# Kernel optimization log

Hardware: AMD Instinct MI355X
Metric: run time of the kernel (lower is better)

## Reference

```python
import jax, jax.numpy as jnp
import numpy as np

N_NODES = 16384
N_EDGES = 32768
D = 128          # node feature / hidden dim
EDGE_DIM = 10    # bond featurizer one-hot dim
EH = 32          # edge_hidden_dim in the NNConv MLPs


def _nnconv(x, src, dst, edge_attr, l1w, l1b, l2w, l2b, root, bias):
    """PyG NNConv with aggr='mean': out_i = x_i @ root + mean_{e: dst=i} x_{src_e} @ W(e) + bias."""
    E = edge_attr.shape[0]
    h = jax.nn.relu(edge_attr @ l1w + l1b)              # [E, EH]
    W = (h @ l2w + l2b).reshape(E, D, D)                # per-edge weight matrices [E, D, D]
    msg = jnp.einsum('ei,eio->eo', x[src], W)           # gather + per-edge matmul [E, D]
    s = jax.ops.segment_sum(msg, dst, num_segments=N_NODES)
    cnt = jax.ops.segment_sum(jnp.ones((E, 1), x.dtype), dst, num_segments=N_NODES)
    agg = s / jnp.maximum(cnt, 1.0)                     # scatter-mean (0 for isolated nodes)
    return x @ root + agg + bias


def setup_inputs() -> dict:
    key = jax.random.key(0)
    ks = jax.random.split(key, 14)
    x = jax.random.normal(ks[0], (N_NODES, D), dtype=jnp.float32)
    edge_index = jax.random.randint(ks[1], (2, N_EDGES), 0, N_NODES, dtype=jnp.int64)
    edge_attr = jax.random.uniform(ks[2], (N_EDGES, EDGE_DIM), dtype=jnp.float32)

    def lin(k, fan_in, fan_out):
        return jax.random.normal(k, (fan_in, fan_out), dtype=jnp.float32) / np.sqrt(fan_in)

    return {
        'x': x, 'edge_index': edge_index, 'edge_attr': edge_attr,
        # subgraph_conv1 (128 -> 128)
        'w1_l1': lin(ks[3], EDGE_DIM, EH), 'b1_l1': jnp.zeros((EH,), jnp.float32),
        'w1_l2': lin(ks[4], EH, D * D),    'b1_l2': jnp.zeros((D * D,), jnp.float32),
        'w1_root': lin(ks[5], D, D),       'b1': jnp.zeros((D,), jnp.float32),
        # subgraph_conv2 (128 -> 128), applied twice with shared weights
        'w2_l1': lin(ks[6], EDGE_DIM, EH), 'b2_l1': jnp.zeros((EH,), jnp.float32),
        'w2_l2': lin(ks[7], EH, D * D),    'b2_l2': jnp.zeros((D * D,), jnp.float32),
        'w2_root': lin(ks[8], D, D),       'b2': jnp.zeros((D,), jnp.float32),
    }


def reference(x, edge_index, edge_attr,
              w1_l1, b1_l1, w1_l2, b1_l2, w1_root, b1,
              w2_l1, b2_l1, w2_l2, b2_l2, w2_root, b2):
    src, dst = edge_index[0], edge_index[1]
    h = jax.nn.relu(_nnconv(x, src, dst, edge_attr, w1_l1, b1_l1, w1_l2, b1_l2, w1_root, b1))
    h = jax.nn.relu(_nnconv(h, src, dst, edge_attr, w2_l1, b2_l1, w2_l2, b2_l2, w2_root, b2))
    h = _nnconv(h, src, dst, edge_attr, w2_l1, b2_l1, w2_l2, b2_l2, w2_root, b2)
    return h
```

## Files before the change

### kernel.cpp

```cpp
#include <hip/hip_runtime.h>

#define N_NODES 16384
#define N_EDGES 32768
#define D 128
#define EDGE_DIM 10
#define KH 32
#define BM 128
#define XST2 72
#define XST 136
#define NBL 32

typedef _Float16 f16;
typedef _Float16 f16x4 __attribute__((ext_vector_type(4)));
typedef _Float16 f16x8 __attribute__((ext_vector_type(8)));
typedef float f32x4 __attribute__((ext_vector_type(4)));

__global__ __launch_bounds__(256) void deg_pack_kernel(
    const int* __restrict__ ei, int* __restrict__ deg,
    const float* __restrict__ w1l2, const float* __restrict__ w2l2,
    const float* __restrict__ b1l2, const float* __restrict__ b2l2,
    const float* __restrict__ rt1, const float* __restrict__ rt2,
    f16* __restrict__ Bp1, f16* __restrict__ Bp2,
    f16* __restrict__ Rp1, f16* __restrict__ Rp2) {
  int y = blockIdx.y;
  if (y == 0) {
    int e = blockIdx.x * 256 + threadIdx.x;
    if (e < N_EDGES) atomicAdd(&deg[ei[N_EDGES + e]], 1);
    return;
  }
  if (blockIdx.x >= D * D / 256) return;
  int t = blockIdx.x * 256 + threadIdx.x;
  int j = y - 1;
  if (j < 2) {
    const float* l2w = j ? w2l2 : w1l2;
    f16* Bp = j ? Bp2 : Bp1;
    f16 tmp[KH];
#pragma unroll
    for (int k = 0; k < KH; k++) tmp[k] = (f16)l2w[(size_t)k * (D * D) + t];
    f16x8* dst = (f16x8*)(Bp + (size_t)t * KH);
#pragma unroll
    for (int c = 0; c < 4; c++) dst[c] = *(f16x8*)&tmp[c * 8];
  } else {
    const float* src = (j == 2) ? b1l2 : (j == 3) ? b2l2 : (j == 4) ? rt1 : rt2;
    f16* dst = (j == 2) ? (Bp1 + (size_t)D * D * KH)
             : (j == 3) ? (Bp2 + (size_t)D * D * KH)
             : (j == 4) ? Rp1 : Rp2;
    int i = t >> 7, o = t & 127;
    dst[((size_t)(i >> 5) * D + o) * KH + (i & 31)] = (f16)src[t];
  }
}

__global__ __launch_bounds__(1024) void scan_kernel(
    const int* __restrict__ deg, int* __restrict__ rs, int* __restrict__ fill) {
  __shared__ int part[1024];
  int t = threadIdx.x;
  int base = t * 16;
  int loc[16], s = 0;
#pragma unroll
  for (int j = 0; j < 16; j++) { loc[j] = deg[base + j]; s += loc[j]; }
  part[t] = s;
  __syncthreads();
  for (int off = 1; off < 1024; off <<= 1) {
    int add = (t >= off) ? part[t - off] : 0;
    __syncthreads();
    part[t] += add;
    __syncthreads();
  }
  int run = t ? part[t - 1] : 0;
#pragma unroll
  for (int j = 0; j < 16; j++) {
    rs[base + j] = run; fill[base + j] = run; run += loc[j];
  }
  if (t == 1023) rs[N_NODES] = run;
}

__global__ __launch_bounds__(256) void scatter_kernel(
    const int* __restrict__ ei, int* __restrict__ fill,
    int* __restrict__ perm, int* __restrict__ srcs) {
  int e = blockIdx.x * blockDim.x + threadIdx.x;
  if (e < N_EDGES) {
    int pos = atomicAdd(&fill[ei[N_EDGES + e]], 1);
    perm[pos] = e;
    srcs[pos] = ei[e];
  }
}

__global__ __launch_bounds__(256) void xcvt_kernel(
    const float* __restrict__ xin, f16* __restrict__ xh) {
  int t = blockIdx.x * 256 + threadIdx.x;
  const float4* s = (const float4*)(xin + (size_t)t * 8);
  float4 v0 = s[0], v1 = s[1];
  f16x8 h = {(f16)v0.x, (f16)v0.y, (f16)v0.z, (f16)v0.w,
             (f16)v1.x, (f16)v1.y, (f16)v1.z, (f16)v1.w};
  *(f16x8*)(xh + (size_t)t * 8) = h;
}

__global__ __launch_bounds__(256) void edge_mlp_kernel(
    const float* __restrict__ ea, const int* __restrict__ perm,
    const float* __restrict__ w1l1, const float* __restrict__ b1l1,
    const float* __restrict__ w2l1, const float* __restrict__ b2l1,
    f16* __restrict__ h1, f16* __restrict__ h2) {
  int p = blockIdx.x * blockDim.x + threadIdx.x;
  const float* l1w = blockIdx.y ? w2l1 : w1l1;
  const float* l1b = blockIdx.y ? b2l1 : b1l1;
  f16* h = blockIdx.y ? h2 : h1;
  int e = perm[p];
  float a[EDGE_DIM];
#pragma unroll
  for (int d = 0; d < EDGE_DIM; d++) a[d] = ea[e * EDGE_DIM + d];
  f16 hv[KH];
#pragma unroll
  for (int k = 0; k < KH; k++) {
    float acc = l1b[k];
#pragma unroll
    for (int d = 0; d < EDGE_DIM; d++) acc += a[d] * l1w[d * KH + k];
    hv[k] = (f16)fmaxf(acc, 0.0f);
  }
  f16x8* dst = (f16x8*)(h + (size_t)p * KH);
#pragma unroll
  for (int c = 0; c < 4; c++) dst[c] = *(f16x8*)&hv[c * 8];
}

__global__ __launch_bounds__(256, 2) void msg_mfma_kernel(
    const f16* __restrict__ xh, const f16* __restrict__ hf,
    const f16* __restrict__ Bp, const int* __restrict__ srcs,
    f16* __restrict__ msgfA, f16* __restrict__ msgfB) {
  __shared__ f16 Xs[BM][XST2];
  __shared__ f16 Hs[BM][KH];
  int t = threadIdx.x;
  int e0 = blockIdx.x * BM;
  int y  = blockIdx.y;
  f16* msgf = y ? msgfB : msgfA;

  ((f16x8*)Hs)[t]       = ((const f16x8*)(hf + (size_t)e0 * KH))[t];
  ((f16x8*)Hs)[t + 256] = ((const f16x8*)(hf + (size_t)e0 * KH))[t + 256];
  {
    int r = t >> 1, q = t & 1;
    int s = srcs[e0 + r];
    const float4* src = (const float4*)(xh + (size_t)s * D + y * 64 + q * 32);
    float4* dst = (float4*)&Xs[r][q * 32];
#pragma unroll
    for (int c = 0; c < 4; c++) dst[c] = src[c];
  }

  int L = t & 63, w = t >> 6;
  int quad = L >> 4, lm = L & 15;
  int n0 = w * 32;

  const f16* bl = Bp + ((size_t)(y * 64) * D + n0 + lm) * KH + quad * 8;
  const size_t istr = (size_t)D * KH;

  f32x4 acc[8][2];
#pragma unroll
  for (int mt = 0; mt < 8; mt++)
#pragma unroll
    for (int nt = 0; nt < 2; nt++)
      acc[mt][nt] = (f32x4){0.f, 0.f, 0.f, 0.f};

  f16x8 bufA[4][2], bufB[4][2];

  auto loadg = [&](f16x8 (&buf)[4][2], int basei) {
#pragma unroll
    for (int jj = 0; jj < 4; jj++) {
      const f16* bi = bl + (size_t)(basei + jj) * istr;
      buf[jj][0] = *(const f16x8*)bi;
      buf[jj][1] = *(const f16x8*)(bi + 16 * KH);
    }
  };

  f16x8 hreg[8];

  auto compute = [&](f16x8 (&buf)[4][2], int ig) {
    f16x4 xv[8];
#pragma unroll
    for (int mt = 0; mt < 8; mt++)
      xv[mt] = *(const f16x4*)&Xs[mt * 16 + lm][ig];
#pragma unroll
    for (int jj = 0; jj < 4; jj++) {
#pragma unroll
      for (int mt = 0; mt < 8; mt++) {
        f16 xs = xv[mt][jj];
        f16x8 xb = {xs, xs, xs, xs, xs, xs, xs, xs};
        f16x8 a = hreg[mt] * xb;
        acc[mt][0] = __builtin_amdgcn_mfma_f32_16x16x32_f16(a, buf[jj][0], acc[mt][0], 0, 0, 0);
        acc[mt][1] = __builtin_amdgcn_mfma_f32_16x16x32_f16(a, buf[jj][1], acc[mt][1], 0, 0, 0);
      }
    }
  };

  loadg(bufA, 0);
  __syncthreads();

#pragma unroll
  for (int mt = 0; mt < 8; mt++)
    hreg[mt] = *(const f16x8*)&Hs[mt * 16 + lm][quad * 8];

#pragma unroll 1
  for (int g = 0; g < 8; g++) {
    loadg(bufB, 8 * g + 4);
    compute(bufA, 8 * g);
    loadg(bufA, 8 * g + 8);
    compute(bufB, 8 * g + 4);
  }

  {
    const f16* bb = Bp + (size_t)D * D * KH;
#pragma unroll
    for (int g2 = 0; g2 < 2; g2++) {
      int ig2 = 2 * y + g2;
      const f16* b2l = bb + ((size_t)ig2 * D + n0 + lm) * KH + quad * 8;
      f16x8 b0 = *(const f16x8*)b2l;
      f16x8 b1 = *(const f16x8*)(b2l + 16 * KH);
      int lc = g2 * 32 + quad * 8;
#pragma unroll
      for (int mt = 0; mt < 8; mt++) {
        f16x8 a = *(const f16x8*)&Xs[mt * 16 + lm][lc];
        acc[mt][0] = __builtin_amdgcn_mfma_f32_16x16x32_f16(a, b0, acc[mt][0], 0, 0, 0);
        acc[mt][1] = __builtin_amdgcn_mfma_f32_16x16x32_f16(a, b1, acc[mt][1], 0, 0, 0);
      }
    }
  }

#pragma unroll
  for (int mt = 0; mt < 8; mt++)
#pragma unroll
    for (int r = 0; r < 4; r++) {
      f16* mg = msgf + (size_t)(e0 + mt * 16 + quad * 4 + r) * D + n0 + lm;
      mg[0]  = (f16)acc[mt][0][r];
      mg[16] = (f16)acc[mt][1][r];
    }
}

__global__ __launch_bounds__(256) void node_update_kernel(
    const f16* __restrict__ xh, const f16* __restrict__ msgA,
    const f16* __restrict__ msgB, const int* __restrict__ rs,
    const f16* __restrict__ Rp, const float* __restrict__ bias,
    f16* __restrict__ xout, float* __restrict__ fout, int is_final) {
  __shared__ f16 Xs[NBL][XST];
  __shared__ float Sls[NBL][D];
  int t = threadIdx.x;
  int nb = blockIdx.x * NBL;

  {
    int r = t >> 3, q = t & 7;
    const float4* src = (const float4*)(xh + (size_t)(nb + r) * D + q * 16);
    float4* dst = (float4*)&Xs[r][q * 16];
    dst[0] = src[0];
    dst[1] = src[1];
  }
  __syncthreads();

  {
    int nl = t >> 3, o0 = (t & 7) * 16;
    int n = nb + nl;
    int a = rs[n], b = rs[n + 1];
    float sum[16];
#pragma unroll
    for (int j = 0; j < 16; j++) sum[j] = 0.f;
    for (int r = a; r < b; r++) {
      f16x8 a0 = *(const f16x8*)(msgA + (size_t)r * D + o0);
      f16x8 a1 = *(const f16x8*)(msgA + (size_t)r * D + o0 + 8);
      f16x8 b0 = *(const f16x8*)(msgB + (size_t)r * D + o0);
      f16x8 b1 = *(const f16x8*)(msgB + (size_t)r * D + o0 + 8);
#pragma unroll
      for (int j = 0; j < 8; j++) {
        sum[j]     += (float)a0[j] + (float)b0[j];
        sum[8 + j] += (float)a1[j] + (float)b1[j];
      }
    }
    float inv = 1.0f / (float)max(b - a, 1);
#pragma unroll
    for (int j = 0; j < 16; j++) Sls[nl][o0 + j] = sum[j] * inv;
  }
  __syncthreads();

  int L = t & 63, w = t >> 6;
  int quad = L >> 4, lm = L & 15;
  int n0 = w * 32;
  f32x4 acc[2][2];
#pragma unroll
  for (int mt = 0; mt < 2; mt++)
#pragma unroll
    for (int nt = 0; nt < 2; nt++)
      acc[mt][nt] = (f32x4){0.f, 0.f, 0.f, 0.f};
#pragma unroll
  for (int s4 = 0; s4 < 4; s4++) {
    const f16* b2l = Rp + ((size_t)s4 * D + n0 + lm) * KH + quad * 8;
    f16x8 b0 = *(const f16x8*)b2l;
    f16x8 b1 = *(const f16x8*)(b2l + 16 * KH);
#pragma unroll
    for (int mt = 0; mt < 2; mt++) {
      f16x8 a = *(const f16x8*)&Xs[mt * 16 + lm][s4 * 32 + quad * 8];
      acc[mt][0] = __builtin_amdgcn_mfma_f32_16x16x32_f16(a, b0, acc[mt][0], 0, 0, 0);
      acc[mt][1] = __builtin_amdgcn_mfma_f32_16x16x32_f16(a, b1, acc[mt][1], 0, 0, 0);
    }
  }
#pragma unroll
  for (int mt = 0; mt < 2; mt++)
#pragma unroll
    for (int r = 0; r < 4; r++) {
      Sls[mt * 16 + quad * 4 + r][n0 + lm] += acc[mt][0][r];
      Sls[mt * 16 + quad * 4 + r][n0 + 16 + lm] += acc[mt][1][r];
    }
  __syncthreads();

  {
    int o = t & 127, g = t >> 7;
    float bo = bias[o];
    if (is_final) {
      for (int q = g * 16; q < g * 16 + 16; q++)
        fout[(size_t)(nb + q) * D + o] = bo + Sls[q][o];
    } else {
      for (int q = g * 16; q < g * 16 + 16; q++)
        xout[(size_t)(nb + q) * D + o] = (f16)fmaxf(bo + Sls[q][o], 0.0f);
    }
  }
}

extern "C" void kernel_launch(void* const* d_in, const int* in_sizes, int n_in,
                              void* d_out, int out_size, void* d_ws, size_t ws_size,
                              hipStream_t stream) {
  const float* x      = (const float*)d_in[0];
  const int*   ei     = (const int*)d_in[1];
  const float* ea     = (const float*)d_in[2];
  const float* w1_l1  = (const float*)d_in[3];
  const float* b1_l1  = (const float*)d_in[4];
  const float* w1_l2  = (const float*)d_in[5];
  const float* b1_l2  = (const float*)d_in[6];
  const float* w1_rt  = (const float*)d_in[7];
  const float* b1     = (const float*)d_in[8];
  const float* w2_l1  = (const float*)d_in[9];
  const float* b2_l1  = (const float*)d_in[10];
  const float* w2_l2  = (const float*)d_in[11];
  const float* b2_l2  = (const float*)d_in[12];
  const float* w2_rt  = (const float*)d_in[13];
  const float* b2     = (const float*)d_in[14];
  float* out = (float*)d_out;

  const size_t BPSZ = (size_t)D * D * KH + (size_t)D * D + 32768;
  f16* h1f = (f16*)d_ws;
  f16* h2f = h1f + (size_t)N_EDGES * KH;
  f16* Bp1 = h2f + (size_t)N_EDGES * KH;
  f16* Bp2 = Bp1 + BPSZ;
  f16* Rp1 = Bp2 + BPSZ;
  f16* Rp2 = Rp1 + (size_t)D * D;
  int* deg  = (int*)(Rp2 + (size_t)D * D);
  int* rs   = deg + N_NODES;
  int* fill = rs + N_NODES + 128;
  int* perm = fill + N_NODES;
  int* srcs = perm + N_EDGES;
  f16* msgA = (f16*)(srcs + N_EDGES);
  f16* msgB = msgA + (size_t)N_EDGES * D;
  f16* xh0  = msgB + (size_t)N_EDGES * D;
  f16* xh1  = xh0 + (size_t)N_NODES * D;

  hipMemsetAsync(deg, 0, N_NODES * sizeof(int), stream);
  deg_pack_kernel<<<dim3(N_EDGES / 256, 7), 256, 0, stream>>>(
      ei, deg, w1_l2, w2_l2, b1_l2, b2_l2, w1_rt, w2_rt, Bp1, Bp2, Rp1, Rp2);
  scan_kernel<<<1, 1024, 0, stream>>>(deg, rs, fill);
  scatter_kernel<<<N_EDGES / 256, 256, 0, stream>>>(ei, fill, perm, srcs);
  edge_mlp_kernel<<<dim3(N_EDGES / 256, 2), 256, 0, stream>>>(
      ea, perm, w1_l1, b1_l1, w2_l1, b2_l1, h1f, h2f);
  xcvt_kernel<<<N_NODES * D / (256 * 8), 256, 0, stream>>>(x, xh0);

  msg_mfma_kernel<<<dim3(N_EDGES / BM, 2), 256, 0, stream>>>(xh0, h1f, Bp1, srcs, msgA, msgB);
  node_update_kernel<<<N_NODES / NBL, 256, 0, stream>>>(xh0, msgA, msgB, rs, Rp1, b1, xh1, out, 0);
  msg_mfma_kernel<<<dim3(N_EDGES / BM, 2), 256, 0, stream>>>(xh1, h2f, Bp2, srcs, msgA, msgB);
  node_update_kernel<<<N_NODES / NBL, 256, 0, stream>>>(xh1, msgA, msgB, rs, Rp2, b2, xh0, out, 0);
  msg_mfma_kernel<<<dim3(N_EDGES / BM, 2), 256, 0, stream>>>(xh0, h2f, Bp2, srcs, msgA, msgB);
  node_update_kernel<<<N_NODES / NBL, 256, 0, stream>>>(xh0, msgA, msgB, rs, Rp2, b2, (f16*)nullptr, out, 1);
}
```

Baseline: 238.7 us.

## Fuse three NNConv layers into a persistent kernel with grid barriers

Replaces the x conversion kernel and the six per-layer message and node-update launches with one persistent kernel of 512 blocks. The blocks step through the phases and meet at atomic-counter grid barriers held in workspace, which is zeroed by the memset. The aim is to remove kernel launch gaps and tail effects between the short phases. It relies on all 512 blocks being resident at the same time (two per CU under the launch bounds), otherwise the barriers deadlock, and each barrier adds spin-wait cost.

```diff
diff --git a/kernel.cpp b/kernel.cpp
--- a/kernel.cpp
+++ b/kernel.cpp
@@ -9,6 +9,8 @@
 #define XST2 72
 #define XST 136
 #define NBL 32
+#define GRID_BLOCKS 512
+#define SMEM_BYTES 26624
 
 typedef _Float16 f16;
 typedef _Float16 f16x4 __attribute__((ext_vector_type(4)));
@@ -85,16 +87,6 @@
   }
 }
 
-__global__ __launch_bounds__(256) void xcvt_kernel(
-    const float* __restrict__ xin, f16* __restrict__ xh) {
-  int t = blockIdx.x * 256 + threadIdx.x;
-  const float4* s = (const float4*)(xin + (size_t)t * 8);
-  float4 v0 = s[0], v1 = s[1];
-  f16x8 h = {(f16)v0.x, (f16)v0.y, (f16)v0.z, (f16)v0.w,
-             (f16)v1.x, (f16)v1.y, (f16)v1.z, (f16)v1.w};
-  *(f16x8*)(xh + (size_t)t * 8) = h;
-}
-
 __global__ __launch_bounds__(256) void edge_mlp_kernel(
     const float* __restrict__ ea, const int* __restrict__ perm,
     const float* __restrict__ w1l1, const float* __restrict__ b1l1,
@@ -121,199 +113,243 @@
   for (int c = 0; c < 4; c++) dst[c] = *(f16x8*)&hv[c * 8];
 }
 
-__global__ __launch_bounds__(256, 2) void msg_mfma_kernel(
-    const f16* __restrict__ xh, const f16* __restrict__ hf,
-    const f16* __restrict__ Bp, const int* __restrict__ srcs,
-    f16* __restrict__ msgfA, f16* __restrict__ msgfB) {
-  __shared__ f16 Xs[BM][XST2];
-  __shared__ f16 Hs[BM][KH];
+__device__ __forceinline__ void grid_barrier(int* bar, int slot) {
+  __syncthreads();
+  if (threadIdx.x == 0) {
+    __threadfence();
+    __hip_atomic_fetch_add(&bar[slot], 1, __ATOMIC_ACQ_REL, __HIP_MEMORY_SCOPE_AGENT);
+    while (__hip_atomic_load(&bar[slot], __ATOMIC_ACQUIRE, __HIP_MEMORY_SCOPE_AGENT)
+           < GRID_BLOCKS)
+      __builtin_amdgcn_s_sleep(2);
+    __threadfence();
+  }
+  __syncthreads();
+}
+
+__global__ __launch_bounds__(256, 2) void fused_layers_kernel(
+    const float* __restrict__ x,
+    const f16* __restrict__ h1f, const f16* __restrict__ h2f,
+    const f16* __restrict__ Bp1, const f16* __restrict__ Bp2,
+    const f16* __restrict__ Rp1, const f16* __restrict__ Rp2,
+    const float* __restrict__ b1, const float* __restrict__ b2,
+    const int* __restrict__ srcs, const int* __restrict__ rs,
+    f16* __restrict__ xh0, f16* __restrict__ xh1,
+    f16* __restrict__ msgA, f16* __restrict__ msgB,
+    float* __restrict__ out, int* bar) {
+  __shared__ __align__(16) char smem[SMEM_BYTES];
   int t = threadIdx.x;
-  int e0 = blockIdx.x * BM;
-  int y  = blockIdx.y;
-  f16* msgf = y ? msgfB : msgfA;
-
-  ((f16x8*)Hs)[t]       = ((const f16x8*)(hf + (size_t)e0 * KH))[t];
-  ((f16x8*)Hs)[t + 256] = ((const f16x8*)(hf + (size_t)e0 * KH))[t + 256];
+  int slot = 0;
+
   {
-    int r = t >> 1, q = t & 1;
-    int s = srcs[e0 + r];
-    const float4* src = (const float4*)(xh + (size_t)s * D + y * 64 + q * 32);
-    float4* dst = (float4*)&Xs[r][q * 32];
-#pragma unroll
-    for (int c = 0; c < 4; c++) dst[c] = src[c];
-  }
-
-  int L = t & 63, w = t >> 6;
-  int quad = L >> 4, lm = L & 15;
-  int n0 = w * 32;
-
-  const f16* bl = Bp + ((size_t)(y * 64) * D + n0 + lm) * KH + quad * 8;
-  const size_t istr = (size_t)D * KH;
-
-  f32x4 acc[8][2];
-#pragma unroll
-  for (int mt = 0; mt < 8; mt++)
-#pragma unroll
-    for (int nt = 0; nt < 2; nt++)
-      acc[mt][nt] = (f32x4){0.f, 0.f, 0.f, 0.f};
-
-  f16x8 bufA[4][2], bufB[4][2];
-
-  auto loadg = [&](f16x8 (&buf)[4][2], int basei) {
-#pragma unroll
-    for (int jj = 0; jj < 4; jj++) {
-      const f16* bi = bl + (size_t)(basei + jj) * istr;
-      buf[jj][0] = *(const f16x8*)bi;
-      buf[jj][1] = *(const f16x8*)(bi + 16 * KH);
+    size_t gid = (size_t)blockIdx.x * 256 + t;
+    const float4* s = (const float4*)(x + gid * 16);
+    float4 v0 = s[0], v1 = s[1], v2 = s[2], v3 = s[3];
+    f16x8 ha = {(f16)v0.x, (f16)v0.y, (f16)v0.z, (f16)v0.w,
+                (f16)v1.x, (f16)v1.y, (f16)v1.z, (f16)v1.w};
+    f16x8 hb = {(f16)v2.x, (f16)v2.y, (f16)v2.z, (f16)v2.w,
+                (f16)v3.x, (f16)v3.y, (f16)v3.z, (f16)v3.w};
+    *(f16x8*)(xh0 + gid * 16) = ha;
+    *(f16x8*)(xh0 + gid * 16 + 8) = hb;
+  }
+  grid_barrier(bar, slot++);
+
+#pragma unroll 1
+  for (int L = 0; L < 3; L++) {
+    const f16* xin = (L == 1) ? xh1 : xh0;
+    f16* xout = (L == 0) ? xh1 : xh0;
+    const f16* hf = L ? h2f : h1f;
+    const f16* Bp = L ? Bp2 : Bp1;
+    const f16* Rp = L ? Rp2 : Rp1;
+    const float* bias = L ? b2 : b1;
+
+    {
+      f16 (*Xs)[XST2] = (f16(*)[XST2])smem;
+      f16 (*Hs)[KH] = (f16(*)[KH])(smem + BM * XST2 * 2);
+      int e0 = (blockIdx.x & 255) * BM;
+      int y = blockIdx.x >> 8;
+      f16* msgf = y ? msgB : msgA;
+
+      ((f16x8*)Hs)[t]       = ((const f16x8*)(hf + (size_t)e0 * KH))[t];
+      ((f16x8*)Hs)[t + 256] = ((const f16x8*)(hf + (size_t)e0 * KH))[t + 256];
+      {
+        int r = t >> 1, q = t & 1;
+        int s = srcs[e0 + r];
+        const float4* src = (const float4*)(xin + (size_t)s * D + y * 64 + q * 32);
+        float4* dst = (float4*)&Xs[r][q * 32];
+#pragma unroll
+        for (int c = 0; c < 4; c++) dst[c] = src[c];
+      }
+
+      int L6 = t & 63, w = t >> 6;
+      int quad = L6 >> 4, lm = L6 & 15;
+      int n0 = w * 32;
+
+      const f16* bl = Bp + ((size_t)(y * 64) * D + n0 + lm) * KH + quad * 8;
+      const size_t istr = (size_t)D * KH;
+
+      f32x4 acc[8][2];
+#pragma unroll
+      for (int mt = 0; mt < 8; mt++)
+#pragma unroll
+        for (int nt = 0; nt < 2; nt++)
+          acc[mt][nt] = (f32x4){0.f, 0.f, 0.f, 0.f};
+
+      f16x8 bufA[4][2], bufB[4][2];
+
+      auto loadg = [&](f16x8 (&buf)[4][2], int basei) {
+#pragma unroll
+        for (int jj = 0; jj < 4; jj++) {
+          const f16* bi = bl + (size_t)(basei + jj) * istr;
+          buf[jj][0] = *(const f16x8*)bi;
+          buf[jj][1] = *(const f16x8*)(bi + 16 * KH);
+        }
+      };
+
+      f16x8 hreg[8];
+
+      auto compute = [&](f16x8 (&buf)[4][2], int ig) {
+        f16x4 xv[8];
+#pragma unroll
+        for (int mt = 0; mt < 8; mt++)
+          xv[mt] = *(const f16x4*)&Xs[mt * 16 + lm][ig];
+#pragma unroll
+        for (int jj = 0; jj < 4; jj++) {
+#pragma unroll
+          for (int mt = 0; mt < 8; mt++) {
+            f16 xs = xv[mt][jj];
+            f16x8 xb = {xs, xs, xs, xs, xs, xs, xs, xs};
+            f16x8 a = hreg[mt] * xb;
+            acc[mt][0] = __builtin_amdgcn_mfma_f32_16x16x32_f16(a, buf[jj][0], acc[mt][0], 0, 0, 0);
+            acc[mt][1] = __builtin_amdgcn_mfma_f32_16x16x32_f16(a, buf[jj][1], acc[mt][1], 0, 0, 0);
+          }
+        }
+      };
+
+      loadg(bufA, 0);
+      __syncthreads();
+
+#pragma unroll
+      for (int mt = 0; mt < 8; mt++)
+        hreg[mt] = *(const f16x8*)&Hs[mt * 16 + lm][quad * 8];
+
+#pragma unroll 1
+      for (int g = 0; g < 8; g++) {
+        loadg(bufB, 8 * g + 4);
+        compute(bufA, 8 * g);
+        loadg(bufA, 8 * g + 8);
+        compute(bufB, 8 * g + 4);
+      }
+
+      {
+        const f16* bb = Bp + (size_t)D * D * KH;
+#pragma unroll
+        for (int g2 = 0; g2 < 2; g2++) {
+          int ig2 = 2 * y + g2;
+          const f16* b2l = bb + ((size_t)ig2 * D + n0 + lm) * KH + quad * 8;
+          f16x8 bb0 = *(const f16x8*)b2l;
+          f16x8 bb1 = *(const f16x8*)(b2l + 16 * KH);
+          int lc = g2 * 32 + quad * 8;
+#pragma unroll
+          for (int mt = 0; mt < 8; mt++) {
+            f16x8 a = *(const f16x8*)&Xs[mt * 16 + lm][lc];
+            acc[mt][0] = __builtin_amdgcn_mfma_f32_16x16x32_f16(a, bb0, acc[mt][0], 0, 0, 0);
+            acc[mt][1] = __builtin_amdgcn_mfma_f32_16x16x32_f16(a, bb1, acc[mt][1], 0, 0, 0);
+          }
+        }
+      }
+
+#pragma unroll
+      for (int mt = 0; mt < 8; mt++)
+#pragma unroll
+        for (int r = 0; r < 4; r++) {
+          f16* mg = msgf + (size_t)(e0 + mt * 16 + quad * 4 + r) * D + n0 + lm;
+          mg[0]  = (f16)acc[mt][0][r];
+          mg[16] = (f16)acc[mt][1][r];
+        }
     }
-  };
-
-  f16x8 hreg[8];
-
-  auto compute = [&](f16x8 (&buf)[4][2], int ig) {
-    f16x4 xv[8];
-#pragma unroll
-    for (int mt = 0; mt < 8; mt++)
-      xv[mt] = *(const f16x4*)&Xs[mt * 16 + lm][ig];
-#pragma unroll
-    for (int jj = 0; jj < 4; jj++) {
-#pragma unroll
-      for (int mt = 0; mt < 8; mt++) {
-        f16 xs = xv[mt][jj];
-        f16x8 xb = {xs, xs, xs, xs, xs, xs, xs, xs};
-        f16x8 a = hreg[mt] * xb;
-        acc[mt][0] = __builtin_amdgcn_mfma_f32_16x16x32_f16(a, buf[jj][0], acc[mt][0], 0, 0, 0);
-        acc[mt][1] = __builtin_amdgcn_mfma_f32_16x16x32_f16(a, buf[jj][1], acc[mt][1], 0, 0, 0);
+    grid_barrier(bar, slot++);
+
+    {
+      f16 (*Xs)[XST] = (f16(*)[XST])smem;
+      float (*Sls)[D] = (float(*)[D])(smem + NBL * XST * 2);
+      int nb = blockIdx.x * NBL;
+
+      {
+        int r = t >> 3, q = t & 7;
+        const float4* src = (const float4*)(xin + (size_t)(nb + r) * D + q * 16);
+        float4* dst = (float4*)&Xs[r][q * 16];
+        dst[0] = src[0];
+        dst[1] = src[1];
+      }
+      __syncthreads();
+
+      {
+        int nl = t >> 3, o0 = (t & 7) * 16;
+        int n = nb + nl;
+        int a = rs[n], b = rs[n + 1];
+        float sum[16];
+#pragma unroll
+        for (int j = 0; j < 16; j++) sum[j] = 0.f;
+        for (int r = a; r < b; r++) {
+          f16x8 a0 = *(const f16x8*)(msgA + (size_t)r * D + o0);
+          f16x8 a1 = *(const f16x8*)(msgA + (size_t)r * D + o0 + 8);
+          f16x8 b0 = *(const f16x8*)(msgB + (size_t)r * D + o0);
+          f16x8 b1 = *(const f16x8*)(msgB + (size_t)r * D + o0 + 8);
+#pragma unroll
+          for (int j = 0; j < 8; j++) {
+            sum[j]     += (float)a0[j] + (float)b0[j];
+            sum[8 + j] += (float)a1[j] + (float)b1[j];
+          }
+        }
+        float inv = 1.0f / (float)max(b - a, 1);
+#pragma unroll
+        for (int j = 0; j < 16; j++) Sls[nl][o0 + j] = sum[j] * inv;
+      }
+      __syncthreads();
+
+      int L6 = t & 63, w = t >> 6;
+      int quad = L6 >> 4, lm = L6 & 15;
+      int n0 = w * 32;
+      f32x4 acc[2][2];
+#pragma unroll
+      for (int mt = 0; mt < 2; mt++)
+#pragma unroll
+        for (int nt = 0; nt < 2; nt++)
+          acc[mt][nt] = (f32x4){0.f, 0.f, 0.f, 0.f};
+#pragma unroll
+      for (int s4 = 0; s4 < 4; s4++) {
+        const f16* b2l = Rp + ((size_t)s4 * D + n0 + lm) * KH + quad * 8;
+        f16x8 rb0 = *(const f16x8*)b2l;
+        f16x8 rb1 = *(const f16x8*)(b2l + 16 * KH);
+#pragma unroll
+        for (int mt = 0; mt < 2; mt++) {
+          f16x8 a = *(const f16x8*)&Xs[mt * 16 + lm][s4 * 32 + quad * 8];
+          acc[mt][0] = __builtin_amdgcn_mfma_f32_16x16x32_f16(a, rb0, acc[mt][0], 0, 0, 0);
+          acc[mt][1] = __builtin_amdgcn_mfma_f32_16x16x32_f16(a, rb1, acc[mt][1], 0, 0, 0);
+        }
+      }
+#pragma unroll
+      for (int mt = 0; mt < 2; mt++)
+#pragma unroll
+        for (int r = 0; r < 4; r++) {
+          Sls[mt * 16 + quad * 4 + r][n0 + lm] += acc[mt][0][r];
+          Sls[mt * 16 + quad * 4 + r][n0 + 16 + lm] += acc[mt][1][r];
+        }
+      __syncthreads();
+
+      {
+        int o = t & 127, g = t >> 7;
+        float bo = bias[o];
+        if (L == 2) {
+          for (int q = g * 16; q < g * 16 + 16; q++)
+            out[(size_t)(nb + q) * D + o] = bo + Sls[q][o];
+        } else {
+          for (int q = g * 16; q < g * 16 + 16; q++)
+            xout[(size_t)(nb + q) * D + o] = (f16)fmaxf(bo + Sls[q][o], 0.0f);
+        }
       }
     }
-  };
-
-  loadg(bufA, 0);
-  __syncthreads();
-
-#pragma unroll
-  for (int mt = 0; mt < 8; mt++)
-    hreg[mt] = *(const f16x8*)&Hs[mt * 16 + lm][quad * 8];
-
-#pragma unroll 1
-  for (int g = 0; g < 8; g++) {
-    loadg(bufB, 8 * g + 4);
-    compute(bufA, 8 * g);
-    loadg(bufA, 8 * g + 8);
-    compute(bufB, 8 * g + 4);
-  }
-
-  {
-    const f16* bb = Bp + (size_t)D * D * KH;
-#pragma unroll
-    for (int g2 = 0; g2 < 2; g2++) {
-      int ig2 = 2 * y + g2;
-      const f16* b2l = bb + ((size_t)ig2 * D + n0 + lm) * KH + quad * 8;
-      f16x8 b0 = *(const f16x8*)b2l;
-      f16x8 b1 = *(const f16x8*)(b2l + 16 * KH);
-      int lc = g2 * 32 + quad * 8;
-#pragma unroll
-      for (int mt = 0; mt < 8; mt++) {
-        f16x8 a = *(const f16x8*)&Xs[mt * 16 + lm][lc];
-        acc[mt][0] = __builtin_amdgcn_mfma_f32_16x16x32_f16(a, b0, acc[mt][0], 0, 0, 0);
-        acc[mt][1] = __builtin_amdgcn_mfma_f32_16x16x32_f16(a, b1, acc[mt][1], 0, 0, 0);
-      }
-    }
-  }
-
-#pragma unroll
-  for (int mt = 0; mt < 8; mt++)
-#pragma unroll
-    for (int r = 0; r < 4; r++) {
-      f16* mg = msgf + (size_t)(e0 + mt * 16 + quad * 4 + r) * D + n0 + lm;
-      mg[0]  = (f16)acc[mt][0][r];
-      mg[16] = (f16)acc[mt][1][r];
-    }
-}
-
-__global__ __launch_bounds__(256) void node_update_kernel(
-    const f16* __restrict__ xh, const f16* __restrict__ msgA,
-    const f16* __restrict__ msgB, const int* __restrict__ rs,
-    const f16* __restrict__ Rp, const float* __restrict__ bias,
-    f16* __restrict__ xout, float* __restrict__ fout, int is_final) {
-  __shared__ f16 Xs[NBL][XST];
-  __shared__ float Sls[NBL][D];
-  int t = threadIdx.x;
-  int nb = blockIdx.x * NBL;
-
-  {
-    int r = t >> 3, q = t & 7;
-    const float4* src = (const float4*)(xh + (size_t)(nb + r) * D + q * 16);
-    float4* dst = (float4*)&Xs[r][q * 16];
-    dst[0] = src[0];
-    dst[1] = src[1];
-  }
-  __syncthreads();
-
-  {
-    int nl = t >> 3, o0 = (t & 7) * 16;
-    int n = nb + nl;
-    int a = rs[n], b = rs[n + 1];
-    float sum[16];
-#pragma unroll
-    for (int j = 0; j < 16; j++) sum[j] = 0.f;
-    for (int r = a; r < b; r++) {
-      f16x8 a0 = *(const f16x8*)(msgA + (size_t)r * D + o0);
-      f16x8 a1 = *(const f16x8*)(msgA + (size_t)r * D + o0 + 8);
-      f16x8 b0 = *(const f16x8*)(msgB + (size_t)r * D + o0);
-      f16x8 b1 = *(const f16x8*)(msgB + (size_t)r * D + o0 + 8);
-#pragma unroll
-      for (int j = 0; j < 8; j++) {
-        sum[j]     += (float)a0[j] + (float)b0[j];
-        sum[8 + j] += (float)a1[j] + (float)b1[j];
-      }
-    }
-    float inv = 1.0f / (float)max(b - a, 1);
-#pragma unroll
-    for (int j = 0; j < 16; j++) Sls[nl][o0 + j] = sum[j] * inv;
-  }
-  __syncthreads();
-
-  int L = t & 63, w = t >> 6;
-  int quad = L >> 4, lm = L & 15;
-  int n0 = w * 32;
-  f32x4 acc[2][2];
-#pragma unroll
-  for (int mt = 0; mt < 2; mt++)
-#pragma unroll
-    for (int nt = 0; nt < 2; nt++)
-      acc[mt][nt] = (f32x4){0.f, 0.f, 0.f, 0.f};
-#pragma unroll
-  for (int s4 = 0; s4 < 4; s4++) {
-    const f16* b2l = Rp + ((size_t)s4 * D + n0 + lm) * KH + quad * 8;
-    f16x8 b0 = *(const f16x8*)b2l;
-    f16x8 b1 = *(const f16x8*)(b2l + 16 * KH);
-#pragma unroll
-    for (int mt = 0; mt < 2; mt++) {
-      f16x8 a = *(const f16x8*)&Xs[mt * 16 + lm][s4 * 32 + quad * 8];
-      acc[mt][0] = __builtin_amdgcn_mfma_f32_16x16x32_f16(a, b0, acc[mt][0], 0, 0, 0);
-      acc[mt][1] = __builtin_amdgcn_mfma_f32_16x16x32_f16(a, b1, acc[mt][1], 0, 0, 0);
-    }
-  }
-#pragma unroll
-  for (int mt = 0; mt < 2; mt++)
-#pragma unroll
-    for (int r = 0; r < 4; r++) {
-      Sls[mt * 16 + quad * 4 + r][n0 + lm] += acc[mt][0][r];
-      Sls[mt * 16 + quad * 4 + r][n0 + 16 + lm] += acc[mt][1][r];
-    }
-  __syncthreads();
-
-  {
-    int o = t & 127, g = t >> 7;
-    float bo = bias[o];
-    if (is_final) {
-      for (int q = g * 16; q < g * 16 + 16; q++)
-        fout[(size_t)(nb + q) * D + o] = bo + Sls[q][o];
-    } else {
-      for (int q = g * 16; q < g * 16 + 16; q++)
-        xout[(size_t)(nb + q) * D + o] = (f16)fmaxf(bo + Sls[q][o], 0.0f);
-    }
+    if (L < 2) grid_barrier(bar, slot++);
   }
 }
 
@@ -345,7 +381,8 @@
   f16* Rp1 = Bp2 + BPSZ;
   f16* Rp2 = Rp1 + (size_t)D * D;
   int* deg  = (int*)(Rp2 + (size_t)D * D);
-  int* rs   = deg + N_NODES;
+  int* bar  = deg + N_NODES;
+  int* rs   = bar + 32;
   int* fill = rs + N_NODES + 128;
   int* perm = fill + N_NODES;
   int* srcs = perm + N_EDGES;
@@ -354,19 +391,15 @@
   f16* xh0  = msgB + (size_t)N_EDGES * D;
   f16* xh1  = xh0 + (size_t)N_NODES * D;
 
-  hipMemsetAsync(deg, 0, N_NODES * sizeof(int), stream);
+  hipMemsetAsync(deg, 0, (N_NODES + 32) * sizeof(int), stream);
   deg_pack_kernel<<<dim3(N_EDGES / 256, 7), 256, 0, stream>>>(
       ei, deg, w1_l2, w2_l2, b1_l2, b2_l2, w1_rt, w2_rt, Bp1, Bp2, Rp1, Rp2);
   scan_kernel<<<1, 1024, 0, stream>>>(deg, rs, fill);
   scatter_kernel<<<N_EDGES / 256, 256, 0, stream>>>(ei, fill, perm, srcs);
   edge_mlp_kernel<<<dim3(N_EDGES / 256, 2), 256, 0, stream>>>(
       ea, perm, w1_l1, b1_l1, w2_l1, b2_l1, h1f, h2f);
-  xcvt_kernel<<<N_NODES * D / (256 * 8), 256, 0, stream>>>(x, xh0);
-
-  msg_mfma_kernel<<<dim3(N_EDGES / BM, 2), 256, 0, stream>>>(xh0, h1f, Bp1, srcs, msgA, msgB);
-  node_update_kernel<<<N_NODES / NBL, 256, 0, stream>>>(xh0, msgA, msgB, rs, Rp1, b1, xh1, out, 0);
-  msg_mfma_kernel<<<dim3(N_EDGES / BM, 2), 256, 0, stream>>>(xh1, h2f, Bp2, srcs, msgA, msgB);
-  node_update_kernel<<<N_NODES / NBL, 256, 0, stream>>>(xh1, msgA, msgB, rs, Rp2, b2, xh0, out, 0);
-  msg_mfma_kernel<<<dim3(N_EDGES / BM, 2), 256, 0, stream>>>(xh0, h2f, Bp2, srcs, msgA, msgB);
-  node_update_kernel<<<N_NODES / NBL, 256, 0, stream>>>(xh0, msgA, msgB, rs, Rp2, b2, (f16*)nullptr, out, 1);
-}
+
+  fused_layers_kernel<<<GRID_BLOCKS, 256, 0, stream>>>(
+      x, h1f, h2f, Bp1, Bp2, Rp1, Rp2, b1, b2, srcs, rs,
+      xh0, xh1, msgA, msgB, out, bar);
+}
```

New measurement: 750.1 us. +214.2%, slower.
